# Optimization experiments

Measured on AMD Instinct MI355X. Metric: run time of the kernel, lower is better.

The kernel has to match this reference:

```python
import math
import jax, jax.numpy as jnp
from jax import lax
import numpy as np

B, CIN, COUT, K, SD, NCLS, H, W = 8, 512, 512, 3, 512, 35, 64, 64
EPS_DEMOD = 1e-8
EPS_IN = 1e-5  # torch InstanceNorm2d default eps


def _equal_linear(x, w, b):
    # EqualLinear: F.linear(x, w * (1/sqrt(in_dim))) + b  (lr_mul=1)
    return x @ (w.T * (1.0 / math.sqrt(w.shape[1]))) + b


def setup_inputs() -> dict:
    key = jax.random.key(0)
    ks = jax.random.split(key, 8)
    return {
        "input": jax.random.normal(ks[0], (B, CIN, H, W), jnp.float32),
        "style": jax.random.normal(ks[1], (B, SD), jnp.float32),
        "class_style": jax.random.normal(ks[2], (NCLS, SD), jnp.float32),
        "weight": jax.random.normal(ks[3], (1, COUT, CIN, K, K), jnp.float32),
        "mod_w": jax.random.normal(ks[4], (CIN, SD), jnp.float32),
        "mod_b": jnp.ones((CIN,), jnp.float32),  # bias_init=1
        "cw_w": jax.random.normal(ks[5], (COUT, SD), jnp.float32),
        "cw_b": jnp.ones((COUT,), jnp.float32),
        "cb_w": jax.random.normal(ks[6], (COUT, SD), jnp.float32),
        "cb_b": jnp.ones((COUT,), jnp.float32),
        "label_class_dict": jax.random.randint(ks[7], (B, H, W), 0, NCLS),
    }


def reference(input, style, class_style, weight, mod_w, mod_b, cw_w, cw_b, cb_w, cb_b, label_class_dict):
    scale = 1.0 / math.sqrt(CIN * K * K)
    pad = K // 2

    # per-sample style modulation of weights
    s = _equal_linear(style, mod_w, mod_b)                 # [B, CIN]
    w = scale * weight * s[:, None, :, None, None]         # [B, COUT, CIN, K, K]
    demod = lax.rsqrt(jnp.sum(w * w, axis=(2, 3, 4)) + EPS_DEMOD)  # [B, COUT]
    w = w * demod[:, :, None, None, None]

    # grouped conv (groups = batch) == vmap of per-sample conv
    def conv_one(x, wb):  # x [CIN,H,W], wb [COUT,CIN,K,K]
        return lax.conv_general_dilated(
            x[None], wb, window_strides=(1, 1), padding=[(pad, pad), (pad, pad)],
            dimension_numbers=("NCHW", "OIHW", "NCHW"))[0]

    out = jax.vmap(conv_one)(input, w)                     # [B, COUT, H, W]

    # param-free instance norm (biased variance, no affine)
    mu = out.mean(axis=(2, 3), keepdims=True)
    var = out.var(axis=(2, 3), keepdims=True)
    out = (out - mu) * lax.rsqrt(var + EPS_IN)

    # CLADE per-class affine from class_style, gathered via label map
    cw = _equal_linear(class_style, cw_w, cw_b)            # [NCLS, COUT]
    cb = _equal_linear(class_style, cb_w, cb_b)            # [NCLS, COUT]
    class_weight = jnp.transpose(cw[label_class_dict], (0, 3, 1, 2))  # [B,COUT,H,W]
    class_bias = jnp.transpose(cb[label_class_dict], (0, 3, 1, 2))
    return out * class_weight + class_bias
```

## Files before the change

kernel.cpp:

```cpp
#include <hip/hip_runtime.h>

typedef unsigned short u16;
typedef unsigned int u32;
typedef __attribute__((ext_vector_type(8))) short short8;
typedef __attribute__((ext_vector_type(4))) float floatx4;

typedef const u32 __attribute__((address_space(1))) glb_u32;
typedef u32 __attribute__((address_space(3))) lds_u32;

__device__ inline float bf2f(u16 h) {
  union { u32 u; float f; } v; v.u = ((u32)h) << 16; return v.f;
}
__device__ inline u16 f2bf(float f) {
  union { float f; u32 u; } v; v.f = f;
  u32 u = v.u;
  return (u16)((u + 0x7fffu + ((u >> 16) & 1u)) >> 16);
}
__device__ inline float ldf(const void* p, int i, int isbf) {
  return isbf ? bf2f(((const u16*)p)[i]) : ((const float*)p)[i];
}
__device__ inline void gl16(const void* g, void* l) {
  __builtin_amdgcn_global_load_lds((glb_u32*)g, (lds_u32*)l, 16, 0, 0);
}

__global__ __launch_bounds__(256) void prep_kernel(
    const void* __restrict__ style, const void* __restrict__ class_style,
    const void* __restrict__ weight,
    const void* __restrict__ mod_w, const void* __restrict__ mod_b,
    const void* __restrict__ cw_w, const void* __restrict__ cw_b,
    const void* __restrict__ cb_w, const void* __restrict__ cb_b,
    const void* __restrict__ x,
    float* __restrict__ s, float* __restrict__ cw, float* __restrict__ cb,
    u16* __restrict__ wT, float* __restrict__ wsqT2, u16* __restrict__ xT) {
  __shared__ float smem[4608];
  __shared__ int cnt;
  const int t = threadIdx.x;

  if (t == 0) cnt = 0;
  __syncthreads();
  {
    u32 v = ((const u32*)weight)[1024 + t];
    int e = (v >> 7) & 0xFF;
    if (e >= 96 && e <= 160) atomicAdd(&cnt, 1);
  }
  __syncthreads();
  const int isbf = (cnt >= 154) ? 1 : 0;
  const int bid = blockIdx.x;

  if (bid < 78) {
    int row = bid;
    const void *vec, *wm, *bias; float* out; int voff;
    if (row < 8)        { vec = style;       voff = row*512;      wm = mod_w; bias = mod_b; out = s  + row*512; }
    else if (row < 43)  { vec = class_style; voff = (row-8)*512;  wm = cw_w;  bias = cw_b;  out = cw + (row-8)*512; }
    else                { vec = class_style; voff = (row-43)*512; wm = cb_w;  bias = cb_b;  out = cb + (row-43)*512; }
    float* v = smem;
    for (int i = t; i < 512; i += 256) v[i] = ldf(vec, voff + i, isbf);
    __syncthreads();
    const float inv = 0.04419417382415922f;
    for (int o = t; o < 512; o += 256) {
      float acc = 0.f;
      if (isbf) {
        for (int k = 0; k < 512; ++k) acc += bf2f(((const u16*)wm)[o*512 + k]) * v[k];
      } else {
        const float4* wr = (const float4*)((const float*)wm + o*512);
        for (int k = 0; k < 128; ++k) {
          float4 p = wr[k];
          acc += p.x*v[k*4+0] + p.y*v[k*4+1] + p.z*v[k*4+2] + p.w*v[k*4+3];
        }
      }
      out[o] = acc * inv + ldf(bias, o, isbf);
    }
  } else if (bid < 590) {
    const int co = bid - 78;
    const int ctb = co >> 6, col = co & 63;
    float* wsmem = smem;
    for (int i = t; i < 4608; i += 256)
      wsmem[i] = ldf(weight, co*4608 + i, isbf);
    __syncthreads();
    for (int ci = t; ci < 512; ci += 256) {
      float sq = 0.f;
      const int ck = ci >> 5, q = (ci >> 3) & 3, e = ci & 7;
      #pragma unroll
      for (int tap = 0; tap < 9; ++tap) {
        float fv = wsmem[ci*9 + tap];
        sq += fv*fv;
        wT[((size_t)(ck*8 + ctb)*2304 + (tap*4 + q)*64 + col)*8 + e] = f2bf(fv);
      }
      wsqT2[(size_t)co*512 + ci] = sq;
    }
  } else {
    const int r = bid - 590;
    const int ck = r & 15, h = (r >> 4) & 63, b = r >> 10;
    float* sv = smem;
    float* sl = smem + 512;
    for (int i = t; i < 512; i += 256) sv[i] = ldf(style, b*512 + i, isbf);
    __syncthreads();
    const int lane = t & 63, wv = t >> 6;
    const float inv = 0.04419417382415922f;
    #pragma unroll
    for (int p = 0; p < 8; ++p) {
      const int row = p*4 + wv;
      const int ci = ck*32 + row;
      float partial = 0.f;
      if (isbf) {
        const u16* wr = (const u16*)mod_w + (size_t)ci*512 + lane*8;
        #pragma unroll
        for (int k = 0; k < 8; ++k) partial += bf2f(wr[k]) * sv[lane*8 + k];
      } else {
        const float4* wr = (const float4*)((const float*)mod_w + (size_t)ci*512 + lane*8);
        float4 p0 = wr[0], p1 = wr[1];
        partial += p0.x*sv[lane*8+0] + p0.y*sv[lane*8+1] + p0.z*sv[lane*8+2] + p0.w*sv[lane*8+3]
                 + p1.x*sv[lane*8+4] + p1.y*sv[lane*8+5] + p1.z*sv[lane*8+6] + p1.w*sv[lane*8+7];
      }
      #pragma unroll
      for (int off = 1; off < 64; off <<= 1) partial += __shfl_xor(partial, off, 64);
      if (lane == 0) sl[row] = partial * inv + ldf(mod_b, ci, isbf);
    }
    __syncthreads();
    const int w = t & 63, cq = t >> 6;
    float f[8];
    #pragma unroll
    for (int j = 0; j < 8; ++j) {
      float xv = ldf(x, (((b*512) + ck*32 + cq*8 + j)*64 + h)*64 + w, isbf);
      f[j] = xv * sl[cq*8 + j];
    }
    u32 outp[4];
    #pragma unroll
    for (int i = 0; i < 4; ++i)
      outp[i] = (u32)f2bf(f[2*i]) | ((u32)f2bf(f[2*i+1]) << 16);
    uint4 po = {outp[0], outp[1], outp[2], outp[3]};
    *(uint4*)&xT[((size_t)(((b*16 + ck)*64 + h)*256) + t)*8] = po;
  }
}

__global__ __launch_bounds__(512, 2) void conv_kernel(const u16* __restrict__ xT, const u16* __restrict__ wT,
                                                      float* __restrict__ y, float* __restrict__ part) {
  __shared__ __align__(16) u16 xs[2*2680*8];
  __shared__ __align__(16) u16 wsm[2*2304*8];
  const int tid = threadIdx.x;
  const int lane = tid & 63;
  const int wid = tid >> 6;
  const int hb = blockIdx.x, b = blockIdx.y;
  const int ctb = blockIdx.z;
  const int ct0 = ctb * 64;
  const int h0 = hb * 8;
  const int m = lane & 15, qd = lane >> 4;

  {
    uint4 z = {0,0,0,0};
    for (int i = tid; i < 5360; i += 512) *(uint4*)&xs[i*8] = z;
  }

  floatx4 acc[4][4];
  #pragma unroll
  for (int i = 0; i < 4; ++i) {
    #pragma unroll
    for (int j = 0; j < 4; ++j) acc[i][j] = (floatx4)(0.f);
  }
  __syncthreads();

  #define STAGE(bn, ckn)                                                                   \
    {                                                                                      \
      u16* xb = &xs[(bn)*21440];                                                           \
      u16* wb = &wsm[(bn)*18432];                                                          \
      for (int sl = wid; sl < 76; sl += 8) {                                               \
        if (sl < 40) {                                                                     \
          int dr = sl >> 2, q = sl & 3;                                                    \
          int hin = h0 + dr - 1;                                                           \
          if (hin >= 0 && hin <= 63) {                                                     \
            const u16* src = xT + ((size_t)(((b*16 + (ckn))*64 + hin)*256 + q*64 + lane))*8;\
            gl16(src, &xb[((dr*4 + q)*67 + 1)*8]);                                         \
          }                                                                                \
        } else {                                                                           \
          int j = sl - 40;                                                                 \
          const u16* src = wT + ((size_t)(((ckn)*8 + ctb)*2304 + j*64 + lane))*8;          \
          gl16(src, &wb[(j*64)*8]);                                                        \
        }                                                                                  \
      }                                                                                    \
    }

  STAGE(0, 0);
  asm volatile("s_waitcnt vmcnt(0)" ::: "memory");
  __syncthreads();

  for (int ck = 0; ck < 16; ++ck) {
    const int buf = ck & 1;
    if (ck < 15) STAGE(buf ^ 1, ck + 1);

    const u16* xb = &xs[buf*21440];
    const u16* wb = &wsm[buf*18432];
    #pragma unroll
    for (int tap = 0; tap < 9; ++tap) {
      const int k1 = tap / 3, k2 = tap - k1*3;
      const int dr = wid + k1;
      short8 af[4], bfr[4];
      #pragma unroll
      for (int mi = 0; mi < 4; ++mi)
        af[mi] = *(const short8*)&wb[((tap*4 + qd)*64 + mi*16 + m)*8];
      #pragma unroll
      for (int nw = 0; nw < 4; ++nw)
        bfr[nw] = *(const short8*)&xb[((dr*4 + qd)*67 + nw*16 + m + k2)*8];
      #pragma unroll
      for (int nw = 0; nw < 4; ++nw) {
        #pragma unroll
        for (int mi = 0; mi < 4; ++mi)
          acc[mi][nw] = __builtin_amdgcn_mfma_f32_16x16x32_bf16(af[mi], bfr[nw], acc[mi][nw], 0, 0, 0);
      }
    }

    asm volatile("s_waitcnt vmcnt(0)" ::: "memory");
    __syncthreads();
  }
  #undef STAGE

  {
    const int h = h0 + wid;
    #pragma unroll
    for (int mi = 0; mi < 4; ++mi) {
      #pragma unroll
      for (int nw = 0; nw < 4; ++nw) {
        #pragma unroll
        for (int r = 0; r < 4; ++r) {
          int co = ct0 + mi*16 + qd*4 + r;
          int w = nw*16 + m;
          y[(size_t)(((b*512) + co)*64 + h)*64 + w] = acc[mi][nw][r];
        }
      }
    }
  }

  float s1[16], s2[16];
  #pragma unroll
  for (int mi = 0; mi < 4; ++mi) {
    #pragma unroll
    for (int r = 0; r < 4; ++r) {
      float a = 0.f, aa = 0.f;
      #pragma unroll
      for (int nw = 0; nw < 4; ++nw) {
        float v = acc[mi][nw][r];
        a += v; aa += v*v;
      }
      s1[mi*4+r] = a; s2[mi*4+r] = aa;
    }
  }
  #pragma unroll
  for (int off = 1; off < 16; off <<= 1) {
    #pragma unroll
    for (int i = 0; i < 16; ++i) {
      s1[i] += __shfl_xor(s1[i], off, 64);
      s2[i] += __shfl_xor(s2[i], off, 64);
    }
  }
  float* red = (float*)xs;
  if (m == 0) {
    #pragma unroll
    for (int mi = 0; mi < 4; ++mi) {
      #pragma unroll
      for (int r = 0; r < 4; ++r) {
        int co = mi*16 + qd*4 + r;
        red[(wid*64 + co)*2 + 0] = s1[mi*4+r];
        red[(wid*64 + co)*2 + 1] = s2[mi*4+r];
      }
    }
  }
  __syncthreads();
  if (tid < 128) {
    int co = tid >> 1, which = tid & 1;
    float v = 0.f;
    #pragma unroll
    for (int w8 = 0; w8 < 8; ++w8) v += red[(w8*64 + co)*2 + which];
    part[(size_t)(((b*8 + hb)*512) + ct0 + co)*2 + which] = v;
  }
}

__global__ __launch_bounds__(256) void epi_kernel(float* __restrict__ y, const float* __restrict__ part,
                                                  const float* __restrict__ s, const float* __restrict__ wsqT2,
                                                  const float* __restrict__ cw, const float* __restrict__ cb,
                                                  const int* __restrict__ label) {
  const int bc = blockIdx.x;
  const int b = bc >> 9, co = bc & 511;
  const int t = threadIdx.x;
  __shared__ float tabw[35], tabb[35];
  __shared__ float redp[4];
  __shared__ float2 msh;
  if (t < 35) { tabw[t] = cw[t*512 + co]; tabb[t] = cb[t*512 + co]; }

  const float* sb = s + b*512;
  const float* wq = wsqT2 + (size_t)co*512;
  float ep;
  {
    float s0 = sb[t], s1v = sb[t + 256];
    ep = s0*s0*wq[t] + s1v*s1v*wq[t + 256];
  }
  #pragma unroll
  for (int off = 1; off < 64; off <<= 1) ep += __shfl_xor(ep, off, 64);
  if ((t & 63) == 0) redp[t >> 6] = ep;
  __syncthreads();
  if (t == 0) {
    float SS = redp[0] + redp[1] + redp[2] + redp[3];
    float S = 0.f, Q = 0.f;
    const float2* pv = (const float2*)part;
    #pragma unroll
    for (int hb = 0; hb < 8; ++hb) {
      float2 p = pv[(size_t)((b*8 + hb)*512) + co];
      S += p.x; Q += p.y;
    }
    float mval = S * (1.f/4096.f);
    float var = fmaxf(Q * (1.f/4096.f) - mval*mval, 0.f);
    float eps = 1e-5f*SS + 4.608e-10f;
    msh = make_float2(mval, rsqrtf(var + eps));
  }
  __syncthreads();
  const float mval = msh.x, is = msh.y;

  float* yp = y + (size_t)bc*4096 + t*16;
  const int* lp = label + b*4096 + t*16;
  #pragma unroll
  for (int u = 0; u < 4; ++u) {
    float4 v = *(const float4*)(yp + u*4);
    int4 l = *(const int4*)(lp + u*4);
    float4 o;
    o.x = (v.x - mval)*is*tabw[l.x] + tabb[l.x];
    o.y = (v.y - mval)*is*tabw[l.y] + tabb[l.y];
    o.z = (v.z - mval)*is*tabw[l.z] + tabb[l.z];
    o.w = (v.w - mval)*is*tabw[l.w] + tabb[l.w];
    *(float4*)(yp + u*4) = o;
  }
}

extern "C" void kernel_launch(void* const* d_in, const int* in_sizes, int n_in,
                              void* d_out, int out_size, void* d_ws, size_t ws_size,
                              hipStream_t stream) {
  (void)in_sizes; (void)n_in; (void)out_size; (void)ws_size;
  const void* input       = d_in[0];
  const void* style       = d_in[1];
  const void* class_style = d_in[2];
  const void* weight      = d_in[3];
  const void* mod_w       = d_in[4];
  const void* mod_b       = d_in[5];
  const void* cw_w        = d_in[6];
  const void* cw_b        = d_in[7];
  const void* cb_w        = d_in[8];
  const void* cb_b        = d_in[9];
  const int* label        = (const int*)d_in[10];
  float* y = (float*)d_out;

  char* ws = (char*)d_ws;
  u16*   xT    = (u16*)  (ws + 0);
  u16*   wT    = (u16*)  (ws + 33554432);
  float* wsqT2 = (float*)(ws + 38273024);
  float* s     = (float*)(ws + 39321600);
  float* cw    = (float*)(ws + 39337984);
  float* cb    = (float*)(ws + 39409664);
  float* part  = (float*)(ws + 39481344);

  hipLaunchKernelGGL(prep_kernel, dim3(8782), dim3(256), 0, stream,
                     style, class_style, weight, mod_w, mod_b, cw_w, cw_b, cb_w, cb_b,
                     input, s, cw, cb, wT, wsqT2, xT);
  hipLaunchKernelGGL(conv_kernel, dim3(8, 8, 8), dim3(512), 0, stream, xT, wT, y, part);
  hipLaunchKernelGGL(epi_kernel, dim3(4096), dim3(256), 0, stream, y, part, s, wsqT2, cw, cb, label);
}
```

Measured before the change: 340.8 us.

## Pad weight LDS rows, double-buffer fragment registers, remap grid to 1D

Weight rows in LDS are padded from 64 to 65 entries to cut bank conflicts on the A-fragment reads. The tap loop is software-pipelined with two register fragment sets, so LDS reads for the next tap overlap the MFMAs of the current one. The 3D grid is flattened to 1D with batch as the fastest index, which changes which blocks run at the same time and may improve L2 reuse of weights and inputs. The extra fragment registers add register pressure at 512 threads with 2 blocks per CU, which could cause spills.

Result: no change. 340.7 us (-0.0%).

```diff
diff --git a/kernel.cpp b/kernel.cpp
--- a/kernel.cpp
+++ b/kernel.cpp
@@ -136,12 +136,12 @@
 __global__ __launch_bounds__(512, 2) void conv_kernel(const u16* __restrict__ xT, const u16* __restrict__ wT,
                                                       float* __restrict__ y, float* __restrict__ part) {
   __shared__ __align__(16) u16 xs[2*2680*8];
-  __shared__ __align__(16) u16 wsm[2*2304*8];
+  __shared__ __align__(16) u16 wsm[2*2340*8];
   const int tid = threadIdx.x;
   const int lane = tid & 63;
   const int wid = tid >> 6;
-  const int hb = blockIdx.x, b = blockIdx.y;
-  const int ctb = blockIdx.z;
+  const int bid = blockIdx.x;
+  const int b = bid & 7, ctb = (bid >> 3) & 7, hb = bid >> 6;
   const int ct0 = ctb * 64;
   const int h0 = hb * 8;
   const int m = lane & 15, qd = lane >> 4;
@@ -162,7 +162,7 @@
   #define STAGE(bn, ckn)                                                                   \
     {                                                                                      \
       u16* xb = &xs[(bn)*21440];                                                           \
-      u16* wb = &wsm[(bn)*18432];                                                          \
+      u16* wb = &wsm[(bn)*18720];                                                          \
       for (int sl = wid; sl < 76; sl += 8) {                                               \
         if (sl < 40) {                                                                     \
           int dr = sl >> 2, q = sl & 3;                                                    \
@@ -174,9 +174,26 @@
         } else {                                                                           \
           int j = sl - 40;                                                                 \
           const u16* src = wT + ((size_t)(((ckn)*8 + ctb)*2304 + j*64 + lane))*8;          \
-          gl16(src, &wb[(j*64)*8]);                                                        \
+          gl16(src, &wb[(j*65)*8]);                                                        \
         }                                                                                  \
       }                                                                                    \
+    }
+
+  #define LOADF(AF, BF, tap)                                                               \
+    {                                                                                      \
+      const int k1c = (tap)/3, k2c = (tap) - k1c*3;                                        \
+      const int drc = wid + k1c;                                                           \
+      _Pragma("unroll") for (int mi = 0; mi < 4; ++mi)                                     \
+        AF[mi] = *(const short8*)&wb[(((tap)*4 + qd)*65 + mi*16 + m)*8];                   \
+      _Pragma("unroll") for (int nw = 0; nw < 4; ++nw)                                     \
+        BF[nw] = *(const short8*)&xb[((drc*4 + qd)*67 + nw*16 + m + k2c)*8];               \
+    }
+
+  #define MFMA16(AF, BF)                                                                   \
+    {                                                                                      \
+      _Pragma("unroll") for (int nw = 0; nw < 4; ++nw)                                     \
+        _Pragma("unroll") for (int mi = 0; mi < 4; ++mi)                                   \
+          acc[mi][nw] = __builtin_amdgcn_mfma_f32_16x16x32_bf16(AF[mi], BF[nw], acc[mi][nw], 0, 0, 0); \
     }
 
   STAGE(0, 0);
@@ -188,30 +205,26 @@
     if (ck < 15) STAGE(buf ^ 1, ck + 1);
 
     const u16* xb = &xs[buf*21440];
-    const u16* wb = &wsm[buf*18432];
-    #pragma unroll
-    for (int tap = 0; tap < 9; ++tap) {
-      const int k1 = tap / 3, k2 = tap - k1*3;
-      const int dr = wid + k1;
-      short8 af[4], bfr[4];
-      #pragma unroll
-      for (int mi = 0; mi < 4; ++mi)
-        af[mi] = *(const short8*)&wb[((tap*4 + qd)*64 + mi*16 + m)*8];
-      #pragma unroll
-      for (int nw = 0; nw < 4; ++nw)
-        bfr[nw] = *(const short8*)&xb[((dr*4 + qd)*67 + nw*16 + m + k2)*8];
-      #pragma unroll
-      for (int nw = 0; nw < 4; ++nw) {
-        #pragma unroll
-        for (int mi = 0; mi < 4; ++mi)
-          acc[mi][nw] = __builtin_amdgcn_mfma_f32_16x16x32_bf16(af[mi], bfr[nw], acc[mi][nw], 0, 0, 0);
-      }
-    }
+    const u16* wb = &wsm[buf*18720];
+    short8 af0[4], bf0[4], af1[4], bf1[4];
+    LOADF(af0, bf0, 0);
+    LOADF(af1, bf1, 1);
+    MFMA16(af0, bf0);  LOADF(af0, bf0, 2);
+    MFMA16(af1, bf1);  LOADF(af1, bf1, 3);
+    MFMA16(af0, bf0);  LOADF(af0, bf0, 4);
+    MFMA16(af1, bf1);  LOADF(af1, bf1, 5);
+    MFMA16(af0, bf0);  LOADF(af0, bf0, 6);
+    MFMA16(af1, bf1);  LOADF(af1, bf1, 7);
+    MFMA16(af0, bf0);  LOADF(af0, bf0, 8);
+    MFMA16(af1, bf1);
+    MFMA16(af0, bf0);
 
     asm volatile("s_waitcnt vmcnt(0)" ::: "memory");
     __syncthreads();
   }
   #undef STAGE
+  #undef LOADF
+  #undef MFMA16
 
   {
     const int h = h0 + wid;
@@ -357,6 +370,6 @@
   hipLaunchKernelGGL(prep_kernel, dim3(8782), dim3(256), 0, stream,
                      style, class_style, weight, mod_w, mod_b, cw_w, cw_b, cb_w, cb_b,
                      input, s, cw, cb, wT, wsqT2, xT);
-  hipLaunchKernelGGL(conv_kernel, dim3(8, 8, 8), dim3(512), 0, stream, xT, wT, y, part);
+  hipLaunchKernelGGL(conv_kernel, dim3(512), dim3(512), 0, stream, xT, wT, y, part);
   hipLaunchKernelGGL(epi_kernel, dim3(4096), dim3(256), 0, stream, y, part, s, wsqT2, cw, cb, label);
 }
```
